# Kernel optimization log

Hardware: AMD Instinct MI355X
Metric: run time of the kernel (lower is better)

Reference implementation:

```python
import jax, jax.numpy as jnp
import numpy as np

N, DIM, K = 262144, 64, 1024

def setup_inputs() -> dict:
    key = jax.random.key(0)
    k1, k2 = jax.random.split(key)
    x = jax.random.normal(k1, (N, DIM), dtype=jnp.float32)
    embed = jax.random.normal(k2, (K, DIM), dtype=jnp.float32)
    return {"x": x, "embed": embed}

def reference(x, embed):
    distances = (jnp.sum(x * x, axis=-1, keepdims=True)
                 - 2.0 * (x @ embed.T)
                 + jnp.sum(embed * embed, axis=-1))  # [N, K]
    idx = jnp.argmin(distances, axis=-1)  # [N]
    # dequantize: embedding lookup
    out = embed[idx]  # [N, DIM]
    return out
```

## Files before the change

### kernel.cpp

```cpp
#include <hip/hip_runtime.h>


#define VQ_N 262144
#define VQ_DIM 64
#define VQ_K 1024
#define NT 64
#define TCH 256
#define FLAG_EPS 1.2e-2f

typedef short short8 __attribute__((ext_vector_type(8)));
typedef float f32x4 __attribute__((ext_vector_type(4)));

#define WS_BFRAG 0
#define WS_E2    (256*1024)
#define WS_E2P   (260*1024)
#define WS_NEEDED (264*1024)

static __device__ __forceinline__ unsigned short f2bf_rtne(float f) {
    unsigned u = __float_as_uint(f);
    unsigned r = u + 0x7FFFu + ((u >> 16) & 1u);
    return (unsigned short)(r >> 16);
}
static __device__ __forceinline__ float bf2f(unsigned short h) {
    return __uint_as_float(((unsigned)h) << 16);
}

__global__ void vq_prep(const float* __restrict__ embed, unsigned char* ws) {
    int t = blockIdx.x * 256 + threadIdx.x;
    if (t < NT * TCH) {
        int ct = t >> 8;
        int c = t & 255;
        int arr = c >> 7;
        int kc = (c >> 6) & 1;
        int l = c & 63;
        int code = ct * 16 + (l & 15);
        int kbase = kc * 32 + ((l >> 4) << 3);
        const float* ep = embed + (size_t)code * VQ_DIM + kbase;
        short8 pack;
#pragma unroll
        for (int j = 0; j < 8; ++j) {
            float v = ep[j];
            unsigned short h = f2bf_rtne(v);
            pack[j] = arr ? (short)f2bf_rtne(v - bf2f(h)) : (short)h;
        }
        ((short8*)(ws + WS_BFRAG))[t] = pack;
    } else if (t < NT * TCH + VQ_K) {
        int code = t - NT * TCH;
        const float* ep = embed + (size_t)code * VQ_DIM;
        float a0 = 0, a1 = 0, a2 = 0, a3 = 0;
#pragma unroll
        for (int j = 0; j < VQ_DIM; j += 4) {
            a0 = fmaf(ep[j], ep[j], a0);
            a1 = fmaf(ep[j + 1], ep[j + 1], a1);
            a2 = fmaf(ep[j + 2], ep[j + 2], a2);
            a3 = fmaf(ep[j + 3], ep[j + 3], a3);
        }
        float e2 = (a0 + a1) + (a2 + a3);
        ((float*)(ws + WS_E2))[code] = e2;
        ((float*)(ws + WS_E2P))[code] = e2 + 256.0f;
    }
}

__global__ __launch_bounds__(256, 4)
void vq_stage1(const float* __restrict__ x, const float* __restrict__ embed,
               unsigned char* ws, float* __restrict__ out) {
    __shared__ int idx_s[4][32];

    const int tid = threadIdx.x;
    const int lane = tid & 63;
    const int wave = tid >> 6;
    const int gwave = blockIdx.x * 4 + wave;
    const int R0 = gwave * 32;
    const int g = lane >> 4;
    const int khalf = g << 3;

    const short8* bsrc = (const short8*)(ws + WS_BFRAG);
    const float* e2g = (const float*)(ws + WS_E2);
    const float* e2p = (const float*)(ws + WS_E2P);

    short8 ah00, ah01, al00, al01, ah10, ah11, al10, al11;
#define MAKE_A(ROW, KC, AH, AL)                                             \
    {                                                                       \
        const float4* p4 = (const float4*)(x + (size_t)(ROW) * VQ_DIM +     \
                                           (KC) * 32 + khalf);              \
        float4 v0 = p4[0], v1 = p4[1];                                      \
        float q0 = -2.0f * v0.x, q1 = -2.0f * v0.y, q2 = -2.0f * v0.z,      \
              q3 = -2.0f * v0.w, q4 = -2.0f * v1.x, q5 = -2.0f * v1.y,      \
              q6 = -2.0f * v1.z, q7 = -2.0f * v1.w;                         \
        unsigned short h0 = f2bf_rtne(q0), h1 = f2bf_rtne(q1),              \
                       h2 = f2bf_rtne(q2), h3 = f2bf_rtne(q3),              \
                       h4 = f2bf_rtne(q4), h5 = f2bf_rtne(q5),              \
                       h6 = f2bf_rtne(q6), h7 = f2bf_rtne(q7);              \
        AH[0] = (short)h0; AH[1] = (short)h1; AH[2] = (short)h2;            \
        AH[3] = (short)h3; AH[4] = (short)h4; AH[5] = (short)h5;            \
        AH[6] = (short)h6; AH[7] = (short)h7;                               \
        AL[0] = (short)f2bf_rtne(q0 - bf2f(h0));                            \
        AL[1] = (short)f2bf_rtne(q1 - bf2f(h1));                            \
        AL[2] = (short)f2bf_rtne(q2 - bf2f(h2));                            \
        AL[3] = (short)f2bf_rtne(q3 - bf2f(h3));                            \
        AL[4] = (short)f2bf_rtne(q4 - bf2f(h4));                            \
        AL[5] = (short)f2bf_rtne(q5 - bf2f(h5));                            \
        AL[6] = (short)f2bf_rtne(q6 - bf2f(h6));                            \
        AL[7] = (short)f2bf_rtne(q7 - bf2f(h7));                            \
    }
    const int row0 = R0 + (lane & 15);
    const int row1 = row0 + 16;
    MAKE_A(row0, 0, ah00, al00)
    MAKE_A(row0, 1, ah01, al01)
    MAKE_A(row1, 0, ah10, al10)
    MAKE_A(row1, 1, ah11, al11)
#undef MAKE_A

    unsigned m1k0[4], m2k0[4], m1k1[4], m2k1[4];
#pragma unroll
    for (int r = 0; r < 4; ++r) {
        m1k0[r] = 0xFFFFFFFFu; m2k0[r] = 0xFFFFFFFFu;
        m1k1[r] = 0xFFFFFFFFu; m2k1[r] = 0xFFFFFFFFu;
    }

#define LOAD_B(CT, B0, B1, B2, B3)                                          \
    {                                                                       \
        const short8* bt = bsrc + (size_t)(CT) * TCH;                       \
        B0 = bt[lane]; B1 = bt[64 + lane];                                  \
        B2 = bt[128 + lane]; B3 = bt[192 + lane];                           \
    }

#define DO_SET(AH0, AH1, AL0, AL1, B0, B1, B2, B3, M1, M2)                            \
    {                                                                                 \
        f32x4 acc = {e2c, e2c, e2c, e2c};                                             \
        acc = __builtin_amdgcn_mfma_f32_16x16x32_bf16(AL0, B0, acc, 0, 0, 0);         \
        acc = __builtin_amdgcn_mfma_f32_16x16x32_bf16(AL1, B1, acc, 0, 0, 0);         \
        acc = __builtin_amdgcn_mfma_f32_16x16x32_bf16(AH0, B2, acc, 0, 0, 0);         \
        acc = __builtin_amdgcn_mfma_f32_16x16x32_bf16(AH1, B3, acc, 0, 0, 0);         \
        acc = __builtin_amdgcn_mfma_f32_16x16x32_bf16(AH0, B0, acc, 0, 0, 0);         \
        acc = __builtin_amdgcn_mfma_f32_16x16x32_bf16(AH1, B1, acc, 0, 0, 0);         \
        _Pragma("unroll")                                                             \
        for (int r = 0; r < 4; ++r) {                                                 \
            unsigned key = (__float_as_uint(acc[r]) & 0xFFFFFFC0u) | ctu;             \
            unsigned t1 = M1[r] > key ? M1[r] : key;                                  \
            M2[r] = M2[r] < t1 ? M2[r] : t1;                                          \
            M1[r] = M1[r] < key ? M1[r] : key;                                        \
        }                                                                             \
    }

#define DO_TILE(CT, B0, B1, B2, B3)                                                   \
    {                                                                                 \
        float e2c = e2p[(CT) * 16 + (lane & 15)];                                     \
        unsigned ctu = (unsigned)(CT);                                                \
        DO_SET(ah00, ah01, al00, al01, B0, B1, B2, B3, m1k0, m2k0)                    \
        DO_SET(ah10, ah11, al10, al11, B0, B1, B2, B3, m1k1, m2k1)                    \
    }

    const int rot = gwave & 63;
    short8 pb0, pb1, pb2, pb3, qb0, qb1, qb2, qb3;
    LOAD_B(rot, pb0, pb1, pb2, pb3)
    for (int it = 0; it < NT; it += 2) {
        const int cte = (rot + it) & 63;
        const int cto = (rot + it + 1) & 63;
        const int ctn = (rot + it + 2) & 63;
        LOAD_B(cto, qb0, qb1, qb2, qb3)
        DO_TILE(cte, pb0, pb1, pb2, pb3)
        LOAD_B(ctn, pb0, pb1, pb2, pb3)
        DO_TILE(cto, qb0, qb1, qb2, qb3)
    }
#undef DO_TILE
#undef DO_SET
#undef LOAD_B

    unsigned res0[4], res1[4];
#pragma unroll
    for (int r = 0; r < 4; ++r) { res0[r] = (unsigned)(lane & 15); res1[r] = res0[r]; }
#define RED_STEP(M1, M2, RES, m)                                                      \
    {                                                                                 \
        _Pragma("unroll")                                                             \
        for (int r = 0; r < 4; ++r) {                                                 \
            unsigned ok = (unsigned)__shfl_xor((int)M1[r], m);                        \
            unsigned ok2 = (unsigned)__shfl_xor((int)M2[r], m);                       \
            unsigned orr = (unsigned)__shfl_xor((int)RES[r], m);                      \
            unsigned t1 = M1[r] > ok ? M1[r] : ok;                                    \
            unsigned c2 = ok2 < t1 ? ok2 : t1;                                        \
            M2[r] = M2[r] < c2 ? M2[r] : c2;                                          \
            bool take = (ok < M1[r]) || (ok == M1[r] && orr < RES[r]);                \
            if (take) { M1[r] = ok; RES[r] = orr; }                                   \
        }                                                                             \
    }
#pragma unroll
    for (int m = 1; m <= 8; m <<= 1) {
        RED_STEP(m1k0, m2k0, res0, m)
        RED_STEP(m1k1, m2k1, res1, m)
    }
#undef RED_STEP

    unsigned fmask = 0;
    if ((lane & 15) == 0) {
#pragma unroll
        for (int r = 0; r < 4; ++r) {
            int rl0 = 4 * g + r;
            idx_s[wave][rl0] = (int)((m1k0[r] & 63u) * 16u + res0[r]);
            float s1 = __uint_as_float(m1k0[r] & 0xFFFFFFC0u);
            float s2 = __uint_as_float(m2k0[r] & 0xFFFFFFC0u);
            if (s2 - s1 < FLAG_EPS) fmask |= 1u << rl0;
            int rl1 = 16 + 4 * g + r;
            idx_s[wave][rl1] = (int)((m1k1[r] & 63u) * 16u + res1[r]);
            float t1f = __uint_as_float(m1k1[r] & 0xFFFFFFC0u);
            float t2f = __uint_as_float(m2k1[r] & 0xFFFFFFC0u);
            if (t2f - t1f < FLAG_EPS) fmask |= 1u << rl1;
        }
    }
    fmask |= (unsigned)__shfl_xor((int)fmask, 16);
    fmask |= (unsigned)__shfl_xor((int)fmask, 32);
    unsigned wmask = (unsigned)__shfl((int)fmask, 0);
    __syncthreads();

    const int orow = tid >> 1;
    const int ohalf = tid & 1;
    int code = idx_s[orow >> 5][orow & 31];
    const float4* ep = (const float4*)(embed + (size_t)code * VQ_DIM) + ohalf * 8;
    float4* op = (float4*)(out + (size_t)(blockIdx.x * 128 + orow) * VQ_DIM) + ohalf * 8;
#pragma unroll
    for (int j = 0; j < 8; ++j) op[j] = ep[j];
    __syncthreads();

    while (wmask) {
        int b = __ffs(wmask) - 1;
        wmask &= wmask - 1;
        int row = R0 + b;
        const float* xr = x + (size_t)row * VQ_DIM;
        float xv[VQ_DIM];
#pragma unroll
        for (int j = 0; j < VQ_DIM / 4; ++j) {
            float4 v = ((const float4*)xr)[j];
            xv[4 * j] = v.x; xv[4 * j + 1] = v.y;
            xv[4 * j + 2] = v.z; xv[4 * j + 3] = v.w;
        }
        float best = __builtin_inff();
        int bi = VQ_K;
        for (int t = 0; t < VQ_K / 64; ++t) {
            int c = t * 64 + lane;
            const float* ep2 = embed + (size_t)c * VQ_DIM;
            float a0 = 0, a1 = 0, a2 = 0, a3 = 0;
#pragma unroll
            for (int j = 0; j < VQ_DIM; j += 4) {
                a0 = fmaf(xv[j], ep2[j], a0);
                a1 = fmaf(xv[j + 1], ep2[j + 1], a1);
                a2 = fmaf(xv[j + 2], ep2[j + 2], a2);
                a3 = fmaf(xv[j + 3], ep2[j + 3], a3);
            }
            float dot = (a0 + a1) + (a2 + a3);
            float s = fmaf(-2.0f, dot, e2g[c]);
            if (s < best || (s == best && c < bi)) { best = s; bi = c; }
        }
#pragma unroll
        for (int m = 1; m <= 32; m <<= 1) {
            float ob = __shfl_xor(best, m);
            int oi = __shfl_xor(bi, m);
            if (ob < best || (ob == best && oi < bi)) { best = ob; bi = oi; }
        }
        out[(size_t)row * VQ_DIM + lane] = embed[(size_t)bi * VQ_DIM + lane];
    }
}

__global__ __launch_bounds__(256, 4)
void vq_fallback(const float* __restrict__ x, const float* __restrict__ embed,
                 float* __restrict__ out) {
    __shared__ float e2s[VQ_K];
    const int tid = threadIdx.x;
    for (int c = tid; c < VQ_K; c += 256) {
        const float4* ep = (const float4*)(embed + c * VQ_DIM);
        float s = 0.0f;
#pragma unroll
        for (int j = 0; j < VQ_DIM / 4; ++j) {
            float4 v = ep[j];
            s = fmaf(v.x, v.x, s); s = fmaf(v.y, v.y, s);
            s = fmaf(v.z, v.z, s); s = fmaf(v.w, v.w, s);
        }
        e2s[c] = s;
    }
    __syncthreads();
    const int row = blockIdx.x * 256 + tid;
    float xr[VQ_DIM];
    const float4* xp = (const float4*)(x + (size_t)row * VQ_DIM);
#pragma unroll
    for (int j = 0; j < VQ_DIM / 4; ++j) {
        float4 v = xp[j];
        xr[4 * j] = v.x; xr[4 * j + 1] = v.y; xr[4 * j + 2] = v.z; xr[4 * j + 3] = v.w;
    }
    float best = __builtin_inff();
    int bidx = 0;
    for (int c = 0; c < VQ_K; ++c) {
        const float4* ep = (const float4*)(embed + c * VQ_DIM);
        float a0 = 0, a1 = 0, a2 = 0, a3 = 0;
#pragma unroll
        for (int j = 0; j < VQ_DIM / 4; ++j) {
            float4 v = ep[j];
            a0 = fmaf(xr[4 * j], v.x, a0);
            a1 = fmaf(xr[4 * j + 1], v.y, a1);
            a2 = fmaf(xr[4 * j + 2], v.z, a2);
            a3 = fmaf(xr[4 * j + 3], v.w, a3);
        }
        float score = fmaf(-2.0f, (a0 + a1) + (a2 + a3), e2s[c]);
        if (score < best) { best = score; bidx = c; }
    }
    const float4* bp = (const float4*)(embed + (size_t)bidx * VQ_DIM);
    float4* op = (float4*)(out + (size_t)row * VQ_DIM);
#pragma unroll
    for (int j = 0; j < VQ_DIM / 4; ++j) op[j] = bp[j];
}

extern "C" void kernel_launch(void* const* d_in, const int* in_sizes, int n_in,
                              void* d_out, int out_size, void* d_ws, size_t ws_size,
                              hipStream_t stream) {
    const float* x = (const float*)d_in[0];
    const float* embed = (const float*)d_in[1];
    float* out = (float*)d_out;
    if (ws_size < WS_NEEDED) {
        hipLaunchKernelGGL(vq_fallback, dim3(VQ_N / 256), dim3(256), 0, stream, x, embed, out);
        return;
    }
    unsigned char* ws = (unsigned char*)d_ws;
    hipLaunchKernelGGL(vq_prep, dim3(68), dim3(256), 0, stream, embed, ws);
    hipLaunchKernelGGL(vq_stage1, dim3(VQ_N / 128), dim3(256), 0, stream, x, embed, ws, out);
}
```

Baseline: 172.8 us.

## Simplify codebook tile loop: drop manual B prefetch, wave rotation and extra barrier

Replaces the hand-written double-buffered B-fragment prefetch and per-wave rotated tile order with a plain loop over codebook tiles, unrolled by two, leaving load scheduling to the compiler. All waves now walk tiles in the same order, which may improve L2/L1 sharing but concentrates accesses on the same lines at the same time. The precomputed e2+256 buffer is removed and the offset is added inline. A __syncthreads after the output copy is also dropped. Together these remove overhead but risk exposing global-load latency in the MFMA loop.

```diff
diff --git a/kernel.cpp b/kernel.cpp
--- a/kernel.cpp
+++ b/kernel.cpp
@@ -13,8 +13,7 @@
 
 #define WS_BFRAG 0
 #define WS_E2    (256*1024)
-#define WS_E2P   (260*1024)
-#define WS_NEEDED (264*1024)
+#define WS_NEEDED (260*1024)
 
 static __device__ __forceinline__ unsigned short f2bf_rtne(float f) {
     unsigned u = __float_as_uint(f);
@@ -55,9 +54,7 @@
             a2 = fmaf(ep[j + 2], ep[j + 2], a2);
             a3 = fmaf(ep[j + 3], ep[j + 3], a3);
         }
-        float e2 = (a0 + a1) + (a2 + a3);
-        ((float*)(ws + WS_E2))[code] = e2;
-        ((float*)(ws + WS_E2P))[code] = e2 + 256.0f;
+        ((float*)(ws + WS_E2))[code] = (a0 + a1) + (a2 + a3);
     }
 }
 
@@ -76,7 +73,6 @@
 
     const short8* bsrc = (const short8*)(ws + WS_BFRAG);
     const float* e2g = (const float*)(ws + WS_E2);
-    const float* e2p = (const float*)(ws + WS_E2P);
 
     short8 ah00, ah01, al00, al01, ah10, ah11, al10, al11;
 #define MAKE_A(ROW, KC, AH, AL)                                             \
@@ -118,54 +114,47 @@
         m1k1[r] = 0xFFFFFFFFu; m2k1[r] = 0xFFFFFFFFu;
     }
 
-#define LOAD_B(CT, B0, B1, B2, B3)                                          \
-    {                                                                       \
-        const short8* bt = bsrc + (size_t)(CT) * TCH;                       \
-        B0 = bt[lane]; B1 = bt[64 + lane];                                  \
-        B2 = bt[128 + lane]; B3 = bt[192 + lane];                           \
-    }
-
-#define DO_SET(AH0, AH1, AL0, AL1, B0, B1, B2, B3, M1, M2)                            \
-    {                                                                                 \
-        f32x4 acc = {e2c, e2c, e2c, e2c};                                             \
-        acc = __builtin_amdgcn_mfma_f32_16x16x32_bf16(AL0, B0, acc, 0, 0, 0);         \
-        acc = __builtin_amdgcn_mfma_f32_16x16x32_bf16(AL1, B1, acc, 0, 0, 0);         \
-        acc = __builtin_amdgcn_mfma_f32_16x16x32_bf16(AH0, B2, acc, 0, 0, 0);         \
-        acc = __builtin_amdgcn_mfma_f32_16x16x32_bf16(AH1, B3, acc, 0, 0, 0);         \
-        acc = __builtin_amdgcn_mfma_f32_16x16x32_bf16(AH0, B0, acc, 0, 0, 0);         \
-        acc = __builtin_amdgcn_mfma_f32_16x16x32_bf16(AH1, B1, acc, 0, 0, 0);         \
-        _Pragma("unroll")                                                             \
-        for (int r = 0; r < 4; ++r) {                                                 \
-            unsigned key = (__float_as_uint(acc[r]) & 0xFFFFFFC0u) | ctu;             \
-            unsigned t1 = M1[r] > key ? M1[r] : key;                                  \
-            M2[r] = M2[r] < t1 ? M2[r] : t1;                                          \
-            M1[r] = M1[r] < key ? M1[r] : key;                                        \
-        }                                                                             \
-    }
-
-#define DO_TILE(CT, B0, B1, B2, B3)                                                   \
-    {                                                                                 \
-        float e2c = e2p[(CT) * 16 + (lane & 15)];                                     \
-        unsigned ctu = (unsigned)(CT);                                                \
-        DO_SET(ah00, ah01, al00, al01, B0, B1, B2, B3, m1k0, m2k0)                    \
-        DO_SET(ah10, ah11, al10, al11, B0, B1, B2, B3, m1k1, m2k1)                    \
-    }
-
-    const int rot = gwave & 63;
-    short8 pb0, pb1, pb2, pb3, qb0, qb1, qb2, qb3;
-    LOAD_B(rot, pb0, pb1, pb2, pb3)
-    for (int it = 0; it < NT; it += 2) {
-        const int cte = (rot + it) & 63;
-        const int cto = (rot + it + 1) & 63;
-        const int ctn = (rot + it + 2) & 63;
-        LOAD_B(cto, qb0, qb1, qb2, qb3)
-        DO_TILE(cte, pb0, pb1, pb2, pb3)
-        LOAD_B(ctn, pb0, pb1, pb2, pb3)
-        DO_TILE(cto, qb0, qb1, qb2, qb3)
-    }
-#undef DO_TILE
-#undef DO_SET
-#undef LOAD_B
+#pragma unroll 2
+    for (int ct = 0; ct < NT; ++ct) {
+        const short8* bt = bsrc + (size_t)ct * TCH;
+        short8 bh0 = bt[lane];
+        short8 bh1 = bt[64 + lane];
+        short8 bl0 = bt[128 + lane];
+        short8 bl1 = bt[192 + lane];
+        float e2c = e2g[ct * 16 + (lane & 15)] + 256.0f;
+        unsigned ctu = (unsigned)ct;
+
+        f32x4 acc0 = {e2c, e2c, e2c, e2c};
+        acc0 = __builtin_amdgcn_mfma_f32_16x16x32_bf16(al00, bh0, acc0, 0, 0, 0);
+        acc0 = __builtin_amdgcn_mfma_f32_16x16x32_bf16(al01, bh1, acc0, 0, 0, 0);
+        acc0 = __builtin_amdgcn_mfma_f32_16x16x32_bf16(ah00, bl0, acc0, 0, 0, 0);
+        acc0 = __builtin_amdgcn_mfma_f32_16x16x32_bf16(ah01, bl1, acc0, 0, 0, 0);
+        acc0 = __builtin_amdgcn_mfma_f32_16x16x32_bf16(ah00, bh0, acc0, 0, 0, 0);
+        acc0 = __builtin_amdgcn_mfma_f32_16x16x32_bf16(ah01, bh1, acc0, 0, 0, 0);
+
+        f32x4 acc1 = {e2c, e2c, e2c, e2c};
+        acc1 = __builtin_amdgcn_mfma_f32_16x16x32_bf16(al10, bh0, acc1, 0, 0, 0);
+        acc1 = __builtin_amdgcn_mfma_f32_16x16x32_bf16(al11, bh1, acc1, 0, 0, 0);
+        acc1 = __builtin_amdgcn_mfma_f32_16x16x32_bf16(ah10, bl0, acc1, 0, 0, 0);
+        acc1 = __builtin_amdgcn_mfma_f32_16x16x32_bf16(ah11, bl1, acc1, 0, 0, 0);
+        acc1 = __builtin_amdgcn_mfma_f32_16x16x32_bf16(ah10, bh0, acc1, 0, 0, 0);
+        acc1 = __builtin_amdgcn_mfma_f32_16x16x32_bf16(ah11, bh1, acc1, 0, 0, 0);
+
+#pragma unroll
+        for (int r = 0; r < 4; ++r) {
+            unsigned key = (__float_as_uint(acc0[r]) & 0xFFFFFFC0u) | ctu;
+            unsigned t1 = m1k0[r] > key ? m1k0[r] : key;
+            m2k0[r] = m2k0[r] < t1 ? m2k0[r] : t1;
+            m1k0[r] = m1k0[r] < key ? m1k0[r] : key;
+        }
+#pragma unroll
+        for (int r = 0; r < 4; ++r) {
+            unsigned key = (__float_as_uint(acc1[r]) & 0xFFFFFFC0u) | ctu;
+            unsigned t1 = m1k1[r] > key ? m1k1[r] : key;
+            m2k1[r] = m2k1[r] < t1 ? m2k1[r] : t1;
+            m1k1[r] = m1k1[r] < key ? m1k1[r] : key;
+        }
+    }
 
     unsigned res0[4], res1[4];
 #pragma unroll
@@ -219,7 +208,6 @@
     float4* op = (float4*)(out + (size_t)(blockIdx.x * 128 + orow) * VQ_DIM) + ohalf * 8;
 #pragma unroll
     for (int j = 0; j < 8; ++j) op[j] = ep[j];
-    __syncthreads();
 
     while (wmask) {
         int b = __ffs(wmask) - 1;
```

Measured after the change: 172.3 us. No clear change (-0.3%).
